# Kernel tuning notes

Hardware: AMD Instinct MI355X
Metric: run time of the kernel (lower is better)

## Reference

```python
import jax, jax.numpy as jnp
import numpy as np

B, L = 32, 96
N = B * L
E = B * L * L
HID, LAT, EEMB = 128, 64, 32
NLAYERS = 3
LAMBDA_CONTRAST = 0.05


def _sinusoidal(t, dim):
    half = dim // 2
    freqs = jnp.exp(-jnp.log(10000.0) * jnp.arange(half, dtype=jnp.float32) / (half - 1))
    ang = t[:, None] * freqs[None, :]
    return jnp.concatenate([jnp.sin(ang), jnp.cos(ang)], axis=-1)


def _forward(H_0, X_0, H_1, X_1, cond_embedding, t_graph,
             Wi1, bi1, Wi2, bi2, Wi3, bi3, edge_table,
             We1, be1, We2, be2, Wx, Wh1, bh1, Wh2, bh2, Wout, bout,
             edges, chain_ids, generate_mask, lengths, shift):
    n = H_0.shape[0]
    b = lengths.shape[0]
    batch_ids = jnp.repeat(jnp.arange(b), lengths, total_repeat_length=n)
    t = t_graph[batch_ids]                      # (N,)
    mask = generate_mask
    mask_f = mask.astype(jnp.float32)

    # path interpolation
    tH = t[:, None]
    H_t = jnp.where(mask[:, None], (1.0 - tH) * H_0 + tH * H_1, H_1)
    X_t = jnp.where(mask[:, None], (1.0 - tH) * X_0 + tH * X_1, X_1)
    v_H_target = H_1 - H_0
    v_X_target = X_1 - X_0

    # edge types from chain-id masking (irregular gather)
    row, col = edges[0], edges[1]
    edge_types = (chain_ids[row] != chain_ids[col]).astype(jnp.int32)

    # --- velocity net ---
    t_embed = _sinusoidal(t, HID)
    h = jnp.concatenate([H_t, cond_embedding, t_embed], axis=-1)
    h = jax.nn.relu(h @ Wi1 + bi1)
    h = jax.nn.relu(h @ Wi2 + bi2)
    h = h @ Wi3 + bi3                            # (N, HID)
    eemb = edge_table[edge_types]                # (E, EEMB)

    X = X_t
    for l in range(NLAYERS):
        rel = X[row] - X[col]                    # (E, 3)
        d2 = jnp.sum(rel * rel, axis=-1, keepdims=True)
        ef = jnp.concatenate([h[row], h[col], d2, eemb], axis=-1)
        m = jax.nn.silu(ef @ We1[l] + be1[l])
        m = jax.nn.silu(m @ We2[l] + be2[l])     # (E, HID)
        coef = m @ Wx[l]                         # (E, 1)
        X = X + jax.ops.segment_sum(rel * coef, row, num_segments=n)
        agg = jax.ops.segment_sum(m, row, num_segments=n)
        hh = jnp.concatenate([h, agg], axis=-1)
        h = h + jax.nn.silu(hh @ Wh1[l] + bh1[l]) @ Wh2[l] + bh2[l]

    v_X_pred = jnp.where(mask[:, None], X, 0.0)
    v_H_pred = jnp.where(mask[:, None], h @ Wout + bout, 0.0)

    # --- losses ---
    msum = mask_f.sum() + 1e-8
    def masked_mse(pred, tgt):
        return (jnp.sum((pred - tgt) ** 2, axis=-1) * mask_f).sum() / msum
    loss_H_pos = masked_mse(v_H_pred, v_H_target)
    loss_X_pos = masked_mse(v_X_pred, v_X_target)

    # negatives: roll over node dim (matches torch indexing (arange+shift)%N)
    v_H_target_neg = jnp.roll(H_1, -shift, axis=0) - jnp.roll(H_0, -shift, axis=0)
    v_X_target_neg = jnp.roll(X_1, -shift, axis=0) - jnp.roll(X_0, -shift, axis=0)
    loss_H_neg = masked_mse(v_H_pred, v_H_target_neg)
    loss_X_neg = masked_mse(v_X_pred, v_X_target_neg)

    loss_H = loss_H_pos - LAMBDA_CONTRAST * loss_H_neg
    loss_X = loss_X_pos - LAMBDA_CONTRAST * loss_X_neg
    return jnp.stack([loss_H, loss_X, loss_H_pos, loss_X_pos, loss_H_neg, loss_X_neg])


def setup_inputs() -> dict:
    key = jax.random.key(0)
    ks = iter(jax.random.split(key, 40))
    def nrm(shape, fan_in):
        return jax.random.normal(next(ks), shape, dtype=jnp.float32) / np.sqrt(fan_in)

    # all-pairs edges within each graph (uniform lengths)
    idx = np.arange(L)
    rb, cb = np.repeat(idx, L), np.tile(idx, L)
    off = (np.arange(B) * L)[:, None]
    rows = (off + rb[None, :]).reshape(-1)
    cols = (off + cb[None, :]).reshape(-1)
    edges = jnp.asarray(np.stack([rows, cols]).astype(np.int32))

    d_in_mlp = LAT + 2 * HID       # 320
    d_in_e = 2 * HID + 1 + EEMB    # 289
    inp = {
        "H_0": jax.random.normal(next(ks), (N, LAT), dtype=jnp.float32),
        "X_0": jax.random.normal(next(ks), (N, 3), dtype=jnp.float32),
        "H_1": jax.random.normal(next(ks), (N, LAT), dtype=jnp.float32),
        "X_1": jax.random.normal(next(ks), (N, 3), dtype=jnp.float32),
        "cond_embedding": jax.random.normal(next(ks), (N, HID), dtype=jnp.float32),
        "t_graph": jax.random.uniform(next(ks), (B,), dtype=jnp.float32),
        "Wi1": nrm((d_in_mlp, HID), d_in_mlp), "bi1": jnp.zeros((HID,)),
        "Wi2": nrm((HID, HID), HID), "bi2": jnp.zeros((HID,)),
        "Wi3": nrm((HID, HID), HID), "bi3": jnp.zeros((HID,)),
        "edge_table": jax.random.normal(next(ks), (2, EEMB), dtype=jnp.float32),
        "We1": nrm((NLAYERS, d_in_e, HID), d_in_e), "be1": jnp.zeros((NLAYERS, HID)),
        "We2": nrm((NLAYERS, HID, HID), HID), "be2": jnp.zeros((NLAYERS, HID)),
        "Wx": nrm((NLAYERS, HID, 1), HID) * 0.01,
        "Wh1": nrm((NLAYERS, 2 * HID, HID), 2 * HID), "bh1": jnp.zeros((NLAYERS, HID)),
        "Wh2": nrm((NLAYERS, HID, HID), HID), "bh2": jnp.zeros((NLAYERS, HID)),
        "Wout": nrm((HID, LAT), HID), "bout": jnp.zeros((LAT,)),
        "edges": edges,
        "chain_ids": jax.random.randint(next(ks), (N,), 0, 3).astype(jnp.int32),
        "generate_mask": jax.random.bernoulli(next(ks), 0.5, (N,)),
        "lengths": jnp.full((B,), L, dtype=jnp.int32),
        "shift": 7,
    }
    return inp


def reference(H_0, X_0, H_1, X_1, cond_embedding, t_graph,
              Wi1, bi1, Wi2, bi2, Wi3, bi3, edge_table,
              We1, be1, We2, be2, Wx, Wh1, bh1, Wh2, bh2, Wout, bout,
              edges, chain_ids, generate_mask, lengths, shift):
    return _forward(H_0, X_0, H_1, X_1, cond_embedding, t_graph,
                    Wi1, bi1, Wi2, bi2, Wi3, bi3, edge_table,
                    We1, be1, We2, be2, Wx, Wh1, bh1, Wh2, bh2, Wout, bout,
                    edges, chain_ids, generate_mask, lengths, shift)
```

## Files before the change

kernel.cpp:

```cpp
#include <hip/hip_runtime.h>
#include <hip/hip_bf16.h>
#include <math.h>

#define NBATCH 32
#define LSEQ   96
#define NN     3072
#define HID    128
#define LAT    64
#define EEMB   32

#define OFF_H      0
#define OFF_X      (OFF_H   + NN*HID)
#define OFF_PA     (OFF_X   + NN*3)
#define OFF_AGG    (OFF_PA  + NN*HID)
#define OFF_DX     (OFF_AGG + NN*HID)
#define OFF_ET     (OFF_DX  + NN*3)
#define OFF_ACC    (OFF_ET  + 768)
#define OFF_NBID   (OFF_ACC + 8)
#define OFF_CUM    (OFF_NBID + NN)
#define OFF_PBH    (OFF_CUM + 40)
#define OFF_BPE    (OFF_PBH + NN*HID/2)
#define OFF_BAB    (OFF_BPE + 24576)
#define OFF_BH1    (OFF_BAB + 49152)
#define OFF_BH2    (OFF_BH1 + 49152)
#define OFF_BWO    (OFF_BH2 + 24576)
#define OFF_BWI1   (OFF_BWO + 4096)
#define OFF_BWI2   (OFF_BWI1 + 20480)
#define OFF_BWI3   (OFF_BWI2 + 8192)
#define OFF_CNT    (OFF_BWI3 + 8192)

typedef short bf16x8 __attribute__((ext_vector_type(8)));
typedef float f32x4  __attribute__((ext_vector_type(4)));

__device__ __forceinline__ short f2bf(float f) {
    unsigned u = __builtin_bit_cast(unsigned, f);
    unsigned r = (u + 0x7FFFu + ((u >> 16) & 1u)) >> 16;
    return (short)r;
}
__device__ __forceinline__ short2 f2bf2(float a, float b) {
    __hip_bfloat162 h = __float22bfloat162_rn(make_float2(a, b));
    short2 r;
    __builtin_memcpy(&r, &h, sizeof(r));
    return r;
}
__device__ __forceinline__ float bf2f(short s) {
    unsigned u = ((unsigned)(unsigned short)s) << 16;
    return __builtin_bit_cast(float, u);
}
__device__ __forceinline__ float silu(float z) {
    return z * __builtin_amdgcn_rcpf(1.0f + __expf(-z));
}

__global__ void k0_all(const float* __restrict__ edge_table, const float* __restrict__ We1,
                       const int* __restrict__ lengths, const float* __restrict__ We2,
                       const float* __restrict__ Wh1, const float* __restrict__ Wh2,
                       const float* __restrict__ Wout, const float* __restrict__ Wi1,
                       const float* __restrict__ Wi2, const float* __restrict__ Wi3,
                       float* __restrict__ ws) {
    int tid = threadIdx.x;
    if (blockIdx.x == 1472) {
        int* cum = (int*)(ws + OFF_CUM);
        int* nb  = (int*)(ws + OFF_NBID);
        float* et = ws + OFF_ET;
        if (tid == 0) {
            int s = 0;
            for (int b = 0; b < NBATCH; b++) { cum[b] = s; s += lengths[b]; }
            cum[NBATCH] = s;
        }
        if (tid < 8) ws[OFF_ACC + tid] = 0.0f;
        if (tid < 128) ((unsigned*)(ws + OFF_CNT))[tid] = 0u;
        __syncthreads();
        for (int i = tid; i < NN; i += blockDim.x) {
            int b = NBATCH - 1;
            for (int q = 0; q < NBATCH; q++) { if (i < cum[q + 1]) { b = q; break; } }
            nb[i] = b;
        }
        for (int idx = tid; idx < 3 * 2 * HID; idx += blockDim.x) {
            int c = idx & 127;
            int t = (idx >> 7) & 1;
            int l = idx >> 8;
            const float* w = We1 + (l * 289 + 257) * HID + c;
            const float* e = edge_table + t * EEMB;
            float s = 0.f;
            for (int k = 0; k < EEMB; k++) s += e[k] * w[k * HID];
            et[idx] = s;
        }
        return;
    }
    int idx = blockIdx.x * 256 + tid;
    short* bpe  = (short*)(ws + OFF_BPE);
    short* bab  = (short*)(ws + OFF_BAB);
    short* bh1  = (short*)(ws + OFF_BH1);
    short* bh2  = (short*)(ws + OFF_BH2);
    short* bwo  = (short*)(ws + OFF_BWO);
    short* bwi1 = (short*)(ws + OFF_BWI1);
    short* bwi2 = (short*)(ws + OFF_BWI2);
    short* bwi3 = (short*)(ws + OFF_BWI3);
    if (idx < 49152) {
        int k = idx & 127, n = (idx >> 7) & 127, l = idx >> 14;
        bpe[idx] = f2bf(We2[(l * 128 + k) * 128 + n]);
    } else if (idx < 147456) {
        int q = idx - 49152;
        int k = q & 127, n = (q >> 7) & 255, l = q >> 15;
        float v = (n < 128) ? We1[(l * 289 + k) * 128 + n]
                            : We1[(l * 289 + 128 + k) * 128 + (n - 128)];
        bab[q] = f2bf(v);
    } else if (idx < 245760) {
        int q = idx - 147456;
        int k = q & 255, n = (q >> 8) & 127, l = q >> 15;
        bh1[q] = f2bf(Wh1[(l * 256 + k) * 128 + n]);
    } else if (idx < 294912) {
        int q = idx - 245760;
        int k = q & 127, n = (q >> 7) & 127, l = q >> 14;
        bh2[q] = f2bf(Wh2[(l * 128 + k) * 128 + n]);
    } else if (idx < 303104) {
        int q = idx - 294912;
        int k = q & 127, n = q >> 7;
        bwo[q] = f2bf(Wout[k * 64 + n]);
    } else if (idx < 344064) {
        int q = idx - 303104;
        int n = q / 320, k = q - n * 320;
        bwi1[q] = f2bf(Wi1[k * 128 + n]);
    } else if (idx < 360448) {
        int q = idx - 344064;
        int k = q & 127, n = q >> 7;
        bwi2[q] = f2bf(Wi2[k * 128 + n]);
    } else if (idx < 376832) {
        int q = idx - 360448;
        int k = q & 127, n = q >> 7;
        bwi3[q] = f2bf(Wi3[k * 128 + n]);
    }
}

__global__ void __launch_bounds__(256)
k1s_node_init(const float* __restrict__ H0, const float* __restrict__ X0,
              const float* __restrict__ H1, const float* __restrict__ X1,
              const float* __restrict__ cond, const float* __restrict__ tg,
              const float* __restrict__ bi1, const float* __restrict__ bi2,
              const float* __restrict__ bi3, const float* __restrict__ be1,
              const int* __restrict__ gmask, float* __restrict__ ws) {
    __shared__ short u1[16 * 136];
    __shared__ short u2[16 * 136];
    int rowbase = blockIdx.x * 96 + blockIdx.y * 16;
    int tid = threadIdx.x;
    int w = tid >> 6, lane = tid & 63;
    int quad = lane >> 4, lp = lane & 15;
    int nodeA = rowbase + lp;
    const int* nb = (const int*)(ws + OFF_NBID);
    float t = tg[nb[nodeA]];
    float u = (gmask[nodeA] != 0) ? t : 1.0f;

    if (tid < 48) {
        int node = rowbase + tid / 3, d = tid % 3;
        float tn = tg[nb[node]];
        float un = (gmask[node] != 0) ? tn : 1.0f;
        ws[OFF_X + (size_t)node * 3 + d] =
            (1.0f - un) * X0[(size_t)node * 3 + d] + un * X1[(size_t)node * 3 + d];
    }

    const short* bwi1 = (const short*)(ws + OFF_BWI1);
    const short* bwi2 = (const short*)(ws + OFF_BWI2);
    const short* bwi3 = (const short*)(ws + OFF_BWI3);
    const short* bab  = (const short*)(ws + OFF_BAB);

    f32x4 acc[2];
    acc[0] = (f32x4){0.f, 0.f, 0.f, 0.f};
    acc[1] = (f32x4){0.f, 0.f, 0.f, 0.f};
    for (int s = 0; s < 10; s++) {
        int kb = s * 32 + quad * 8;
        float z[8];
        if (kb < 64) {
            const float* h0 = H0 + (size_t)nodeA * 64 + kb;
            const float* h1 = H1 + (size_t)nodeA * 64 + kb;
            #pragma unroll
            for (int e = 0; e < 8; e++) z[e] = (1.0f - u) * h0[e] + u * h1[e];
        } else if (kb < 192) {
            const float* cp = cond + (size_t)nodeA * 128 + (kb - 64);
            #pragma unroll
            for (int e = 0; e < 8; e++) z[e] = cp[e];
        } else if (kb < 256) {
            #pragma unroll
            for (int e = 0; e < 8; e++) {
                float c = (float)(kb - 192 + e);
                float fr = __expf(-9.2103403719761836f * c / 63.0f);
                z[e] = __sinf(t * fr);
            }
        } else {
            #pragma unroll
            for (int e = 0; e < 8; e++) {
                float c = (float)(kb - 256 + e);
                float fr = __expf(-9.2103403719761836f * c / 63.0f);
                z[e] = __cosf(t * fr);
            }
        }
        bf16x8 af;
        #pragma unroll
        for (int e = 0; e < 8; e += 2) {
            short2 p = f2bf2(z[e], z[e + 1]);
            af[e] = p.x; af[e + 1] = p.y;
        }
        #pragma unroll
        for (int i = 0; i < 2; i++) {
            int ct = 2 * w + i;
            bf16x8 bf = *(const bf16x8*)(bwi1 + (size_t)(16 * ct + lp) * 320 + kb);
            acc[i] = __builtin_amdgcn_mfma_f32_16x16x32_bf16(af, bf, acc[i], 0, 0, 0);
        }
    }
    #pragma unroll
    for (int i = 0; i < 2; i++) {
        int ch = 16 * (2 * w + i) + lp;
        float bb1 = bi1[ch];
        #pragma unroll
        for (int r = 0; r < 4; r++)
            u1[(quad * 4 + r) * 136 + ch] = f2bf(fmaxf(acc[i][r] + bb1, 0.0f));
    }
    __syncthreads();

    acc[0] = (f32x4){0.f, 0.f, 0.f, 0.f};
    acc[1] = (f32x4){0.f, 0.f, 0.f, 0.f};
    #pragma unroll
    for (int s = 0; s < 4; s++) {
        int kb = s * 32 + quad * 8;
        bf16x8 af = *(const bf16x8*)(u1 + lp * 136 + kb);
        #pragma unroll
        for (int i = 0; i < 2; i++) {
            int ct = 2 * w + i;
            bf16x8 bf = *(const bf16x8*)(bwi2 + (size_t)(16 * ct + lp) * 128 + kb);
            acc[i] = __builtin_amdgcn_mfma_f32_16x16x32_bf16(af, bf, acc[i], 0, 0, 0);
        }
    }
    #pragma unroll
    for (int i = 0; i < 2; i++) {
        int ch = 16 * (2 * w + i) + lp;
        float bb2 = bi2[ch];
        #pragma unroll
        for (int r = 0; r < 4; r++)
            u2[(quad * 4 + r) * 136 + ch] = f2bf(fmaxf(acc[i][r] + bb2, 0.0f));
    }
    __syncthreads();

    acc[0] = (f32x4){0.f, 0.f, 0.f, 0.f};
    acc[1] = (f32x4){0.f, 0.f, 0.f, 0.f};
    #pragma unroll
    for (int s = 0; s < 4; s++) {
        int kb = s * 32 + quad * 8;
        bf16x8 af = *(const bf16x8*)(u2 + lp * 136 + kb);
        #pragma unroll
        for (int i = 0; i < 2; i++) {
            int ct = 2 * w + i;
            bf16x8 bf = *(const bf16x8*)(bwi3 + (size_t)(16 * ct + lp) * 128 + kb);
            acc[i] = __builtin_amdgcn_mfma_f32_16x16x32_bf16(af, bf, acc[i], 0, 0, 0);
        }
    }
    #pragma unroll
    for (int i = 0; i < 2; i++) {
        int ch = 16 * (2 * w + i) + lp;
        float bb3 = bi3[ch];
        #pragma unroll
        for (int r = 0; r < 4; r++) {
            int row = quad * 4 + r;
            float h = acc[i][r] + bb3;
            ws[OFF_H + (size_t)(rowbase + row) * 128 + ch] = h;
            u1[row * 136 + ch] = f2bf(h);
        }
    }
    __syncthreads();

    f32x4 acc4[4];
    #pragma unroll
    for (int i = 0; i < 4; i++) acc4[i] = (f32x4){0.f, 0.f, 0.f, 0.f};
    #pragma unroll
    for (int s = 0; s < 4; s++) {
        int kb = s * 32 + quad * 8;
        bf16x8 af = *(const bf16x8*)(u1 + lp * 136 + kb);
        #pragma unroll
        for (int i = 0; i < 4; i++) {
            int ct4 = 4 * w + i;
            bf16x8 bf = *(const bf16x8*)(bab + (size_t)(16 * ct4 + lp) * 128 + kb);
            acc4[i] = __builtin_amdgcn_mfma_f32_16x16x32_bf16(af, bf, acc4[i], 0, 0, 0);
        }
    }
    short* pbh = (short*)(ws + OFF_PBH);
    #pragma unroll
    for (int i = 0; i < 4; i++) {
        int ct4 = 4 * w + i;
        #pragma unroll
        for (int r = 0; r < 4; r++) {
            int node = rowbase + quad * 4 + r;
            if (ct4 < 8) {
                int ch = 16 * ct4 + lp;
                ws[OFF_PA + (size_t)node * 128 + ch] = acc4[i][r] + be1[ch];
            } else {
                int ch = 16 * (ct4 - 8) + lp;
                pbh[(size_t)node * 128 + ch] = f2bf(acc4[i][r]);
            }
        }
    }
}

#define KG 4
#define SMC_BS    0
#define SMC_AGG   32768
#define SMC_PA    35840
#define SMC_ET    37888
#define SMC_WC    38912
#define SMC_COEF  39424
#define SMC_XT    39808
#define SMC_CI    39856
__global__ void __launch_bounds__(384)
k3c_edge(const float* __restrict__ We1, const float* __restrict__ Wx,
         const float* __restrict__ be2, const int* __restrict__ chain,
         int l, float* __restrict__ ws) {
    __shared__ __align__(16) char smem[39872];
    short* bS    = (short*)(smem + SMC_BS);
    float* aggP  = (float*)(smem + SMC_AGG);
    float* paS   = (float*)(smem + SMC_PA);
    float* etS   = (float*)(smem + SMC_ET);
    float* wcS   = (float*)(smem + SMC_WC);
    float* coefS = (float*)(smem + SMC_COEF);
    float* xT    = (float*)(smem + SMC_XT);
    int*   ciS   = (int*)  (smem + SMC_CI);

    int tid = threadIdx.x;
    int i0 = blockIdx.x * KG;
    int colbase = (i0 / 96) * 96;
    const float* Xc = ws + OFF_X;

    {
        const short* bpe = (const short*)(ws + OFF_BPE) + (size_t)l * 128 * 128;
        for (int idx = tid; idx < 2048; idx += 384) {
            int t = idx >> 8, s = (idx >> 6) & 3, ln = idx & 63;
            int lq = ln >> 4, lpp = ln & 15;
            *(bf16x8*)(bS + idx * 8) =
                *(const bf16x8*)(bpe + (size_t)(16 * t + lpp) * 128 + s * 32 + lq * 8);
        }
        if (tid < 128) {
            #pragma unroll
            for (int g = 0; g < KG; g++)
                paS[g * 128 + tid] = ws[OFF_PA + (size_t)(i0 + g) * 128 + tid];
            etS[tid]       = ws[OFF_ET + l * 256 + tid];
            etS[128 + tid] = ws[OFF_ET + l * 256 + 128 + tid];
            wcS[tid]       = We1[(l * 289 + 256) * 128 + tid];
        }
        if (tid < KG * 3) xT[tid] = Xc[(size_t)(i0 + tid / 3) * 3 + tid % 3];
        if (tid < KG) ciS[tid] = chain[i0 + tid];
    }

    int w = tid >> 6, lane = tid & 63;
    int quad = lane >> 4, lp = lane & 15;
    int jA = 16 * w + lp;
    const short* pbrow = (const short*)(ws + OFF_PBH) + (size_t)(colbase + jA) * 128;
    bf16x8 pbv[4];
    #pragma unroll
    for (int s = 0; s < 4; s++) pbv[s] = *(const bf16x8*)(pbrow + s * 32 + quad * 8);
    float xr0 = Xc[(size_t)(colbase + jA) * 3 + 0];
    float xr1 = Xc[(size_t)(colbase + jA) * 3 + 1];
    float xr2 = Xc[(size_t)(colbase + jA) * 3 + 2];
    int cj = chain[colbase + jA];
    float be2r[8], wxr[8];
    #pragma unroll
    for (int t = 0; t < 8; t++) {
        int ch = 16 * t + lp;
        be2r[t] = be2[l * 128 + ch];
        wxr[t]  = Wx[l * 128 + ch];
    }
    float ex0 = 0.f, ex1 = 0.f;
    if (w < 3) {
        ex0 = Xc[(size_t)(colbase + lane) * 3 + w];
        if (lane < 32) ex1 = Xc[(size_t)(colbase + lane + 64) * 3 + w];
    }
    __syncthreads();

    for (int g = 0; g < KG; g++) {
        float rx = xT[g * 3 + 0] - xr0;
        float ry = xT[g * 3 + 1] - xr1;
        float rz = xT[g * 3 + 2] - xr2;
        float d2j = rx * rx + ry * ry + rz * rz;
        const float* etP = etS + ((cj != ciS[g]) ? 128 : 0);
        const float* paP = paS + g * 128;

        f32x4 acc[8];
        #pragma unroll
        for (int t = 0; t < 8; t++) acc[t] = (f32x4){0.f, 0.f, 0.f, 0.f};

        #pragma unroll
        for (int s = 0; s < 4; s++) {
            int kb = s * 32 + quad * 8;
            float z[8];
            #pragma unroll
            for (int e = 0; e < 8; e++)
                z[e] = silu(paP[kb + e] + etP[kb + e] + bf2f(pbv[s][e]) + d2j * wcS[kb + e]);
            bf16x8 af;
            #pragma unroll
            for (int e = 0; e < 8; e += 2) {
                short2 p = f2bf2(z[e], z[e + 1]);
                af[e] = p.x; af[e + 1] = p.y;
            }
            #pragma unroll
            for (int t = 0; t < 8; t++) {
                bf16x8 bf = *(const bf16x8*)(bS + ((t * 4 + s) * 64 + lane) * 8);
                acc[t] = __builtin_amdgcn_mfma_f32_16x16x32_bf16(af, bf, acc[t], 0, 0, 0);
            }
        }

        float cp[4] = {0.f, 0.f, 0.f, 0.f};
        #pragma unroll
        for (int t = 0; t < 8; t++) {
            float ag = 0.f;
            #pragma unroll
            for (int r = 0; r < 4; r++) {
                float m2 = silu(acc[t][r] + be2r[t]);
                ag += m2;
                cp[r] += m2 * wxr[t];
            }
            ag += __shfl_xor(ag, 16);
            ag += __shfl_xor(ag, 32);
            if (lane < 16) aggP[w * 128 + 16 * t + lp] = ag;
        }
        #pragma unroll
        for (int r = 0; r < 4; r++) {
            float v = cp[r];
            v += __shfl_xor(v, 1);
            v += __shfl_xor(v, 2);
            v += __shfl_xor(v, 4);
            v += __shfl_xor(v, 8);
            if (lp == 0) coefS[16 * w + quad * 4 + r] = v;
        }
        __syncthreads();

        if (tid < 128) {
            float s = 0.f;
            #pragma unroll
            for (int q = 0; q < 6; q++) s += aggP[q * 128 + tid];
            ws[OFF_AGG + (size_t)(i0 + g) * 128 + tid] = s;
        }
        if (w < 3) {
            float v = (xT[g * 3 + w] - ex0) * coefS[lane];
            if (lane < 32) v += (xT[g * 3 + w] - ex1) * coefS[lane + 64];
            #pragma unroll
            for (int o = 32; o > 0; o >>= 1) v += __shfl_down(v, o);
            if (lane == 0) ws[OFF_DX + (size_t)(i0 + g) * 3 + w] = v;
        }
        __syncthreads();
    }
}

__global__ void __launch_bounds__(256)
k4s_node_post(const float* __restrict__ bh1, const float* __restrict__ bh2,
              const float* __restrict__ be1, const float* __restrict__ bout,
              const float* __restrict__ H0, const float* __restrict__ X0,
              const float* __restrict__ H1, const float* __restrict__ X1,
              const int* __restrict__ gmask, const int* __restrict__ shiftp,
              int l, float* __restrict__ ws, float* __restrict__ out) {
    __shared__ short uS[16 * 136];
    __shared__ short hS[16 * 136];
    __shared__ float redE[4], redN[4];
    __shared__ float sxp, sxn, scnt;
    int rowbase = blockIdx.x * 96 + blockIdx.y * 16;
    int tid = threadIdx.x;
    int w = tid >> 6, lane = tid & 63;
    int quad = lane >> 4, lp = lane & 15;
    int nodeA = rowbase + lp;
    const short* b1 = (const short*)(ws + OFF_BH1) + (size_t)l * 128 * 256;
    const short* b2 = (const short*)(ws + OFF_BH2) + (size_t)l * 128 * 128;

    if (tid == 0) { sxp = 0.f; sxn = 0.f; scnt = 0.f; }
    if (tid < 48) {
        int node = rowbase + tid / 3, d = tid % 3;
        ws[OFF_X + (size_t)node * 3 + d] += ws[OFF_DX + (size_t)node * 3 + d];
    }

    f32x4 acc[2];
    acc[0] = (f32x4){0.f, 0.f, 0.f, 0.f};
    acc[1] = (f32x4){0.f, 0.f, 0.f, 0.f};
    #pragma unroll
    for (int s = 0; s < 8; s++) {
        int kb = s * 32 + quad * 8;
        const float* src = (kb < 128) ? (ws + OFF_H + (size_t)nodeA * 128 + kb)
                                      : (ws + OFF_AGG + (size_t)nodeA * 128 + (kb - 128));
        bf16x8 af;
        #pragma unroll
        for (int e = 0; e < 8; e += 2) {
            short2 p = f2bf2(src[e], src[e + 1]);
            af[e] = p.x; af[e + 1] = p.y;
        }
        #pragma unroll
        for (int i = 0; i < 2; i++) {
            int ct = 2 * w + i;
            bf16x8 bf = *(const bf16x8*)(b1 + (size_t)(16 * ct + lp) * 256 + kb);
            acc[i] = __builtin_amdgcn_mfma_f32_16x16x32_bf16(af, bf, acc[i], 0, 0, 0);
        }
    }
    #pragma unroll
    for (int i = 0; i < 2; i++) {
        int ch = 16 * (2 * w + i) + lp;
        float bb1 = bh1[l * 128 + ch];
        #pragma unroll
        for (int r = 0; r < 4; r++)
            uS[(quad * 4 + r) * 136 + ch] = f2bf(silu(acc[i][r] + bb1));
    }
    __syncthreads();

    acc[0] = (f32x4){0.f, 0.f, 0.f, 0.f};
    acc[1] = (f32x4){0.f, 0.f, 0.f, 0.f};
    #pragma unroll
    for (int s = 0; s < 4; s++) {
        int kb = s * 32 + quad * 8;
        bf16x8 af = *(const bf16x8*)(uS + lp * 136 + kb);
        #pragma unroll
        for (int i = 0; i < 2; i++) {
            int ct = 2 * w + i;
            bf16x8 bf = *(const bf16x8*)(b2 + (size_t)(16 * ct + lp) * 128 + kb);
            acc[i] = __builtin_amdgcn_mfma_f32_16x16x32_bf16(af, bf, acc[i], 0, 0, 0);
        }
    }
    #pragma unroll
    for (int i = 0; i < 2; i++) {
        int ch = 16 * (2 * w + i) + lp;
        float bb2 = bh2[l * 128 + ch];
        #pragma unroll
        for (int r = 0; r < 4; r++) {
            int row = quad * 4 + r;
            size_t off = OFF_H + (size_t)(rowbase + row) * 128 + ch;
            float h = ws[off] + acc[i][r] + bb2;
            ws[off] = h;
            hS[row * 136 + ch] = f2bf(h);
        }
    }
    __syncthreads();

    if (l < 2) {
        const short* bab = (const short*)(ws + OFF_BAB) + (size_t)(l + 1) * 256 * 128;
        f32x4 acc4[4];
        #pragma unroll
        for (int i = 0; i < 4; i++) acc4[i] = (f32x4){0.f, 0.f, 0.f, 0.f};
        #pragma unroll
        for (int s = 0; s < 4; s++) {
            int kb = s * 32 + quad * 8;
            bf16x8 af = *(const bf16x8*)(hS + lp * 136 + kb);
            #pragma unroll
            for (int i = 0; i < 4; i++) {
                int ct4 = 4 * w + i;
                bf16x8 bf = *(const bf16x8*)(bab + (size_t)(16 * ct4 + lp) * 128 + kb);
                acc4[i] = __builtin_amdgcn_mfma_f32_16x16x32_bf16(af, bf, acc4[i], 0, 0, 0);
            }
        }
        short* pbh = (short*)(ws + OFF_PBH);
        #pragma unroll
        for (int i = 0; i < 4; i++) {
            int ct4 = 4 * w + i;
            #pragma unroll
            for (int r = 0; r < 4; r++) {
                int node = rowbase + quad * 4 + r;
                if (ct4 < 8) {
                    int ch = 16 * ct4 + lp;
                    ws[OFF_PA + (size_t)node * 128 + ch] = acc4[i][r] + be1[(l + 1) * 128 + ch];
                } else {
                    int ch = 16 * (ct4 - 8) + lp;
                    pbh[(size_t)node * 128 + ch] = f2bf(acc4[i][r]);
                }
            }
        }
    } else {
        const short* bwo = (const short*)(ws + OFF_BWO);
        f32x4 accv = (f32x4){0.f, 0.f, 0.f, 0.f};
        #pragma unroll
        for (int s = 0; s < 4; s++) {
            int kb = s * 32 + quad * 8;
            bf16x8 af = *(const bf16x8*)(hS + lp * 136 + kb);
            bf16x8 bf = *(const bf16x8*)(bwo + (size_t)(16 * w + lp) * 128 + kb);
            accv = __builtin_amdgcn_mfma_f32_16x16x32_bf16(af, bf, accv, 0, 0, 0);
        }
        int s = shiftp[0] % NN; if (s < 0) s += NN;
        int col = 16 * w + lp;
        float bo = bout[col];
        float ep = 0.f, en = 0.f;
        #pragma unroll
        for (int r = 0; r < 4; r++) {
            int row = rowbase + quad * 4 + r;
            if (gmask[row] != 0) {
                int ip = row + s; if (ip >= NN) ip -= NN;
                float v  = accv[r] + bo;
                float tp = H1[(size_t)row * 64 + col] - H0[(size_t)row * 64 + col];
                float tn = H1[(size_t)ip * 64 + col]  - H0[(size_t)ip * 64 + col];
                float dp = v - tp, dn = v - tn;
                ep += dp * dp;
                en += dn * dn;
            }
        }
        #pragma unroll
        for (int o = 1; o < 64; o <<= 1) {
            ep += __shfl_xor(ep, o);
            en += __shfl_xor(en, o);
        }
        if (lane == 0) { redE[w] = ep; redN[w] = en; }

        if (tid < 16) {
            int node = rowbase + tid;
            if (gmask[node] != 0) {
                int ip = node + s; if (ip >= NN) ip -= NN;
                float xp = 0.f, xn = 0.f;
                #pragma unroll
                for (int d = 0; d < 3; d++) {
                    float xv  = ws[OFF_X + (size_t)node * 3 + d];
                    float tpx = X1[(size_t)node * 3 + d] - X0[(size_t)node * 3 + d];
                    float tnx = X1[(size_t)ip * 3 + d]   - X0[(size_t)ip * 3 + d];
                    xp += (xv - tpx) * (xv - tpx);
                    xn += (xv - tnx) * (xv - tnx);
                }
                atomicAdd(&sxp, xp);
                atomicAdd(&sxn, xn);
                atomicAdd(&scnt, 1.0f);
            }
        }
        __syncthreads();
        if (tid == 0) {
            float eT = redE[0] + redE[1] + redE[2] + redE[3];
            float nT = redN[0] + redN[1] + redN[2] + redN[3];
            float* acc0 = ws + OFF_ACC;
            atomicAdd(acc0 + 0, eT);
            atomicAdd(acc0 + 2, nT);
            atomicAdd(acc0 + 1, sxp);
            atomicAdd(acc0 + 3, sxn);
            atomicAdd(acc0 + 4, scnt);
            __threadfence();
            unsigned o2 = atomicAdd((unsigned*)(ws + OFF_CNT) + 96, 1u);
            if (o2 == 191u) {
                __threadfence();
                float a0 = atomicAdd(acc0 + 0, 0.0f);
                float a1 = atomicAdd(acc0 + 1, 0.0f);
                float a2 = atomicAdd(acc0 + 2, 0.0f);
                float a3 = atomicAdd(acc0 + 3, 0.0f);
                float a4 = atomicAdd(acc0 + 4, 0.0f);
                float msum = a4 + 1e-8f;
                float lhp = a0 / msum, lxp = a1 / msum;
                float lhn = a2 / msum, lxn = a3 / msum;
                out[0] = lhp - 0.05f * lhn;
                out[1] = lxp - 0.05f * lxn;
                out[2] = lhp;
                out[3] = lxp;
                out[4] = lhn;
                out[5] = lxn;
            }
        }
    }
}

extern "C" void kernel_launch(void* const* d_in, const int* in_sizes, int n_in,
                              void* d_out, int out_size, void* d_ws, size_t ws_size,
                              hipStream_t stream) {
    (void)in_sizes; (void)n_in; (void)out_size; (void)ws_size;
    const float* H0   = (const float*)d_in[0];
    const float* X0   = (const float*)d_in[1];
    const float* H1   = (const float*)d_in[2];
    const float* X1   = (const float*)d_in[3];
    const float* cond = (const float*)d_in[4];
    const float* tg   = (const float*)d_in[5];
    const float* Wi1  = (const float*)d_in[6];
    const float* bi1  = (const float*)d_in[7];
    const float* Wi2  = (const float*)d_in[8];
    const float* bi2  = (const float*)d_in[9];
    const float* Wi3  = (const float*)d_in[10];
    const float* bi3  = (const float*)d_in[11];
    const float* etab = (const float*)d_in[12];
    const float* We1  = (const float*)d_in[13];
    const float* be1  = (const float*)d_in[14];
    const float* We2  = (const float*)d_in[15];
    const float* be2  = (const float*)d_in[16];
    const float* Wx   = (const float*)d_in[17];
    const float* Wh1  = (const float*)d_in[18];
    const float* bh1  = (const float*)d_in[19];
    const float* Wh2  = (const float*)d_in[20];
    const float* bh2  = (const float*)d_in[21];
    const float* Wout = (const float*)d_in[22];
    const float* bout = (const float*)d_in[23];
    const int* chain   = (const int*)d_in[25];
    const int* gmask   = (const int*)d_in[26];
    const int* lengths = (const int*)d_in[27];
    const int* shiftp  = (const int*)d_in[28];
    float* ws  = (float*)d_ws;
    float* out = (float*)d_out;

    k0_all<<<1473, 256, 0, stream>>>(etab, We1, lengths, We2, Wh1, Wh2,
                                     Wout, Wi1, Wi2, Wi3, ws);
    k1s_node_init<<<dim3(NBATCH, 6), 256, 0, stream>>>(H0, X0, H1, X1, cond, tg,
                                                       bi1, bi2, bi3, be1, gmask, ws);
    for (int l = 0; l < 3; l++) {
        k3c_edge<<<NN / KG, 384, 0, stream>>>(We1, Wx, be2, chain, l, ws);
        k4s_node_post<<<dim3(NBATCH, 6), 256, 0, stream>>>(bh1, bh2, be1, bout,
                                                           H0, X0, H1, X1, gmask, shiftp,
                                                           l, ws, out);
    }
}
```

Before: 389.7 us.

## Interleave two target nodes per edge MFMA pass and widen node-post kernel to 8 waves

The edge kernel now handles two destination nodes at once, issuing paired MFMAs that share each B-fragment load from LDS, and moves be2/Wx from per-thread registers into shared memory. The node-post kernel runs 512 threads (8 waves), so each wave computes one 16-column tile instead of two. In the final layer only the first four waves do the output projection. The aim is more instruction-level parallelism and less register pressure per wave, at the cost of doubled accumulator registers in the edge kernel and extra LDS reads.

```diff
diff --git a/kernel.cpp b/kernel.cpp
--- a/kernel.cpp
+++ b/kernel.cpp
@@ -304,19 +304,23 @@
 #define SMC_PA    35840
 #define SMC_ET    37888
 #define SMC_WC    38912
-#define SMC_COEF  39424
-#define SMC_XT    39808
-#define SMC_CI    39856
+#define SMC_BE2   39424
+#define SMC_WX    39936
+#define SMC_COEF  40448
+#define SMC_XT    40832
+#define SMC_CI    40880
 __global__ void __launch_bounds__(384)
-k3c_edge(const float* __restrict__ We1, const float* __restrict__ Wx,
-         const float* __restrict__ be2, const int* __restrict__ chain,
-         int l, float* __restrict__ ws) {
-    __shared__ __align__(16) char smem[39872];
+k3c2_edge(const float* __restrict__ We1, const float* __restrict__ Wx,
+          const float* __restrict__ be2, const int* __restrict__ chain,
+          int l, float* __restrict__ ws) {
+    __shared__ __align__(16) char smem[40896];
     short* bS    = (short*)(smem + SMC_BS);
     float* aggP  = (float*)(smem + SMC_AGG);
     float* paS   = (float*)(smem + SMC_PA);
     float* etS   = (float*)(smem + SMC_ET);
     float* wcS   = (float*)(smem + SMC_WC);
+    float* be2S  = (float*)(smem + SMC_BE2);
+    float* wxS   = (float*)(smem + SMC_WX);
     float* coefS = (float*)(smem + SMC_COEF);
     float* xT    = (float*)(smem + SMC_XT);
     int*   ciS   = (int*)  (smem + SMC_CI);
@@ -341,6 +345,8 @@
             etS[tid]       = ws[OFF_ET + l * 256 + tid];
             etS[128 + tid] = ws[OFF_ET + l * 256 + 128 + tid];
             wcS[tid]       = We1[(l * 289 + 256) * 128 + tid];
+            be2S[tid]      = be2[l * 128 + tid];
+            wxS[tid]       = Wx[l * 128 + tid];
         }
         if (tid < KG * 3) xT[tid] = Xc[(size_t)(i0 + tid / 3) * 3 + tid % 3];
         if (tid < KG) ciS[tid] = chain[i0 + tid];
@@ -357,13 +363,6 @@
     float xr1 = Xc[(size_t)(colbase + jA) * 3 + 1];
     float xr2 = Xc[(size_t)(colbase + jA) * 3 + 2];
     int cj = chain[colbase + jA];
-    float be2r[8], wxr[8];
-    #pragma unroll
-    for (int t = 0; t < 8; t++) {
-        int ch = 16 * t + lp;
-        be2r[t] = be2[l * 128 + ch];
-        wxr[t]  = Wx[l * 128 + ch];
-    }
     float ex0 = 0.f, ex1 = 0.f;
     if (w < 3) {
         ex0 = Xc[(size_t)(colbase + lane) * 3 + w];
@@ -371,90 +370,109 @@
     }
     __syncthreads();
 
-    for (int g = 0; g < KG; g++) {
-        float rx = xT[g * 3 + 0] - xr0;
-        float ry = xT[g * 3 + 1] - xr1;
-        float rz = xT[g * 3 + 2] - xr2;
-        float d2j = rx * rx + ry * ry + rz * rz;
-        const float* etP = etS + ((cj != ciS[g]) ? 128 : 0);
-        const float* paP = paS + g * 128;
-
-        f32x4 acc[8];
-        #pragma unroll
-        for (int t = 0; t < 8; t++) acc[t] = (f32x4){0.f, 0.f, 0.f, 0.f};
+    for (int gp = 0; gp < KG; gp += 2) {
+        int gA = gp, gB = gp + 1;
+        float rxA = xT[gA * 3 + 0] - xr0, ryA = xT[gA * 3 + 1] - xr1, rzA = xT[gA * 3 + 2] - xr2;
+        float rxB = xT[gB * 3 + 0] - xr0, ryB = xT[gB * 3 + 1] - xr1, rzB = xT[gB * 3 + 2] - xr2;
+        float d2A = rxA * rxA + ryA * ryA + rzA * rzA;
+        float d2B = rxB * rxB + ryB * ryB + rzB * rzB;
+        const float* etA = etS + ((cj != ciS[gA]) ? 128 : 0);
+        const float* etB = etS + ((cj != ciS[gB]) ? 128 : 0);
+        const float* paA = paS + gA * 128;
+        const float* paB = paS + gB * 128;
+
+        f32x4 accA[8], accB[8];
+        #pragma unroll
+        for (int t = 0; t < 8; t++) {
+            accA[t] = (f32x4){0.f, 0.f, 0.f, 0.f};
+            accB[t] = (f32x4){0.f, 0.f, 0.f, 0.f};
+        }
 
         #pragma unroll
         for (int s = 0; s < 4; s++) {
             int kb = s * 32 + quad * 8;
-            float z[8];
-            #pragma unroll
-            for (int e = 0; e < 8; e++)
-                z[e] = silu(paP[kb + e] + etP[kb + e] + bf2f(pbv[s][e]) + d2j * wcS[kb + e]);
-            bf16x8 af;
+            bf16x8 afA, afB;
             #pragma unroll
             for (int e = 0; e < 8; e += 2) {
-                short2 p = f2bf2(z[e], z[e + 1]);
-                af[e] = p.x; af[e + 1] = p.y;
+                float pb0 = bf2f(pbv[s][e]), pb1 = bf2f(pbv[s][e + 1]);
+                float wc0 = wcS[kb + e], wc1 = wcS[kb + e + 1];
+                float zA0 = silu(paA[kb + e]     + etA[kb + e]     + pb0 + d2A * wc0);
+                float zA1 = silu(paA[kb + e + 1] + etA[kb + e + 1] + pb1 + d2A * wc1);
+                float zB0 = silu(paB[kb + e]     + etB[kb + e]     + pb0 + d2B * wc0);
+                float zB1 = silu(paB[kb + e + 1] + etB[kb + e + 1] + pb1 + d2B * wc1);
+                short2 pA = f2bf2(zA0, zA1);
+                short2 pB = f2bf2(zB0, zB1);
+                afA[e] = pA.x; afA[e + 1] = pA.y;
+                afB[e] = pB.x; afB[e + 1] = pB.y;
             }
             #pragma unroll
             for (int t = 0; t < 8; t++) {
                 bf16x8 bf = *(const bf16x8*)(bS + ((t * 4 + s) * 64 + lane) * 8);
-                acc[t] = __builtin_amdgcn_mfma_f32_16x16x32_bf16(af, bf, acc[t], 0, 0, 0);
-            }
-        }
-
-        float cp[4] = {0.f, 0.f, 0.f, 0.f};
-        #pragma unroll
-        for (int t = 0; t < 8; t++) {
-            float ag = 0.f;
+                accA[t] = __builtin_amdgcn_mfma_f32_16x16x32_bf16(afA, bf, accA[t], 0, 0, 0);
+                accB[t] = __builtin_amdgcn_mfma_f32_16x16x32_bf16(afB, bf, accB[t], 0, 0, 0);
+            }
+        }
+
+        #pragma unroll
+        for (int half = 0; half < 2; half++) {
+            int g = (half == 0) ? gA : gB;
+            f32x4* acc = (half == 0) ? accA : accB;
+            float cp[4] = {0.f, 0.f, 0.f, 0.f};
+            #pragma unroll
+            for (int t = 0; t < 8; t++) {
+                int ch = 16 * t + lp;
+                float bb = be2S[ch];
+                float wx = wxS[ch];
+                float ag = 0.f;
+                #pragma unroll
+                for (int r = 0; r < 4; r++) {
+                    float m2 = silu(acc[t][r] + bb);
+                    ag += m2;
+                    cp[r] += m2 * wx;
+                }
+                ag += __shfl_xor(ag, 16);
+                ag += __shfl_xor(ag, 32);
+                if (lane < 16) aggP[w * 128 + ch] = ag;
+            }
             #pragma unroll
             for (int r = 0; r < 4; r++) {
-                float m2 = silu(acc[t][r] + be2r[t]);
-                ag += m2;
-                cp[r] += m2 * wxr[t];
-            }
-            ag += __shfl_xor(ag, 16);
-            ag += __shfl_xor(ag, 32);
-            if (lane < 16) aggP[w * 128 + 16 * t + lp] = ag;
-        }
-        #pragma unroll
-        for (int r = 0; r < 4; r++) {
-            float v = cp[r];
-            v += __shfl_xor(v, 1);
-            v += __shfl_xor(v, 2);
-            v += __shfl_xor(v, 4);
-            v += __shfl_xor(v, 8);
-            if (lp == 0) coefS[16 * w + quad * 4 + r] = v;
-        }
-        __syncthreads();
-
-        if (tid < 128) {
-            float s = 0.f;
-            #pragma unroll
-            for (int q = 0; q < 6; q++) s += aggP[q * 128 + tid];
-            ws[OFF_AGG + (size_t)(i0 + g) * 128 + tid] = s;
-        }
-        if (w < 3) {
-            float v = (xT[g * 3 + w] - ex0) * coefS[lane];
-            if (lane < 32) v += (xT[g * 3 + w] - ex1) * coefS[lane + 64];
-            #pragma unroll
-            for (int o = 32; o > 0; o >>= 1) v += __shfl_down(v, o);
-            if (lane == 0) ws[OFF_DX + (size_t)(i0 + g) * 3 + w] = v;
-        }
-        __syncthreads();
-    }
-}
-
-__global__ void __launch_bounds__(256)
-k4s_node_post(const float* __restrict__ bh1, const float* __restrict__ bh2,
-              const float* __restrict__ be1, const float* __restrict__ bout,
-              const float* __restrict__ H0, const float* __restrict__ X0,
-              const float* __restrict__ H1, const float* __restrict__ X1,
-              const int* __restrict__ gmask, const int* __restrict__ shiftp,
-              int l, float* __restrict__ ws, float* __restrict__ out) {
+                float v = cp[r];
+                v += __shfl_xor(v, 1);
+                v += __shfl_xor(v, 2);
+                v += __shfl_xor(v, 4);
+                v += __shfl_xor(v, 8);
+                if (lp == 0) coefS[16 * w + quad * 4 + r] = v;
+            }
+            __syncthreads();
+
+            if (tid < 128) {
+                float s = 0.f;
+                #pragma unroll
+                for (int q = 0; q < 6; q++) s += aggP[q * 128 + tid];
+                ws[OFF_AGG + (size_t)(i0 + g) * 128 + tid] = s;
+            }
+            if (w < 3) {
+                float v = (xT[g * 3 + w] - ex0) * coefS[lane];
+                if (lane < 32) v += (xT[g * 3 + w] - ex1) * coefS[lane + 64];
+                #pragma unroll
+                for (int o = 32; o > 0; o >>= 1) v += __shfl_down(v, o);
+                if (lane == 0) ws[OFF_DX + (size_t)(i0 + g) * 3 + w] = v;
+            }
+            __syncthreads();
+        }
+    }
+}
+
+__global__ void __launch_bounds__(512)
+k4s8_node_post(const float* __restrict__ bh1, const float* __restrict__ bh2,
+               const float* __restrict__ be1, const float* __restrict__ bout,
+               const float* __restrict__ H0, const float* __restrict__ X0,
+               const float* __restrict__ H1, const float* __restrict__ X1,
+               const int* __restrict__ gmask, const int* __restrict__ shiftp,
+               int l, float* __restrict__ ws, float* __restrict__ out) {
     __shared__ short uS[16 * 136];
     __shared__ short hS[16 * 136];
-    __shared__ float redE[4], redN[4];
+    __shared__ float redE[8], redN[8];
     __shared__ float sxp, sxn, scnt;
     int rowbase = blockIdx.x * 96 + blockIdx.y * 16;
     int tid = threadIdx.x;
@@ -470,9 +488,7 @@
         ws[OFF_X + (size_t)node * 3 + d] += ws[OFF_DX + (size_t)node * 3 + d];
     }
 
-    f32x4 acc[2];
-    acc[0] = (f32x4){0.f, 0.f, 0.f, 0.f};
-    acc[1] = (f32x4){0.f, 0.f, 0.f, 0.f};
+    f32x4 acc = (f32x4){0.f, 0.f, 0.f, 0.f};
     #pragma unroll
     for (int s = 0; s < 8; s++) {
         int kb = s * 32 + quad * 8;
@@ -484,45 +500,34 @@
             short2 p = f2bf2(src[e], src[e + 1]);
             af[e] = p.x; af[e + 1] = p.y;
         }
-        #pragma unroll
-        for (int i = 0; i < 2; i++) {
-            int ct = 2 * w + i;
-            bf16x8 bf = *(const bf16x8*)(b1 + (size_t)(16 * ct + lp) * 256 + kb);
-            acc[i] = __builtin_amdgcn_mfma_f32_16x16x32_bf16(af, bf, acc[i], 0, 0, 0);
-        }
-    }
-    #pragma unroll
-    for (int i = 0; i < 2; i++) {
-        int ch = 16 * (2 * w + i) + lp;
+        bf16x8 bf = *(const bf16x8*)(b1 + (size_t)(16 * w + lp) * 256 + kb);
+        acc = __builtin_amdgcn_mfma_f32_16x16x32_bf16(af, bf, acc, 0, 0, 0);
+    }
+    {
+        int ch = 16 * w + lp;
         float bb1 = bh1[l * 128 + ch];
         #pragma unroll
         for (int r = 0; r < 4; r++)
-            uS[(quad * 4 + r) * 136 + ch] = f2bf(silu(acc[i][r] + bb1));
+            uS[(quad * 4 + r) * 136 + ch] = f2bf(silu(acc[r] + bb1));
     }
     __syncthreads();
 
-    acc[0] = (f32x4){0.f, 0.f, 0.f, 0.f};
-    acc[1] = (f32x4){0.f, 0.f, 0.f, 0.f};
+    acc = (f32x4){0.f, 0.f, 0.f, 0.f};
     #pragma unroll
     for (int s = 0; s < 4; s++) {
         int kb = s * 32 + quad * 8;
         bf16x8 af = *(const bf16x8*)(uS + lp * 136 + kb);
-        #pragma unroll
-        for (int i = 0; i < 2; i++) {
-            int ct = 2 * w + i;
-            bf16x8 bf = *(const bf16x8*)(b2 + (size_t)(16 * ct + lp) * 128 + kb);
-            acc[i] = __builtin_amdgcn_mfma_f32_16x16x32_bf16(af, bf, acc[i], 0, 0, 0);
-        }
-    }
-    #pragma unroll
-    for (int i = 0; i < 2; i++) {
-        int ch = 16 * (2 * w + i) + lp;
+        bf16x8 bf = *(const bf16x8*)(b2 + (size_t)(16 * w + lp) * 128 + kb);
+        acc = __builtin_amdgcn_mfma_f32_16x16x32_bf16(af, bf, acc, 0, 0, 0);
+    }
+    {
+        int ch = 16 * w + lp;
         float bb2 = bh2[l * 128 + ch];
         #pragma unroll
         for (int r = 0; r < 4; r++) {
             int row = quad * 4 + r;
             size_t off = OFF_H + (size_t)(rowbase + row) * 128 + ch;
-            float h = ws[off] + acc[i][r] + bb2;
+            float h = ws[off] + acc[r] + bb2;
             ws[off] = h;
             hS[row * 136 + ch] = f2bf(h);
         }
@@ -531,24 +536,24 @@
 
     if (l < 2) {
         const short* bab = (const short*)(ws + OFF_BAB) + (size_t)(l + 1) * 256 * 128;
-        f32x4 acc4[4];
-        #pragma unroll
-        for (int i = 0; i < 4; i++) acc4[i] = (f32x4){0.f, 0.f, 0.f, 0.f};
+        f32x4 acc4[2];
+        acc4[0] = (f32x4){0.f, 0.f, 0.f, 0.f};
+        acc4[1] = (f32x4){0.f, 0.f, 0.f, 0.f};
         #pragma unroll
         for (int s = 0; s < 4; s++) {
             int kb = s * 32 + quad * 8;
             bf16x8 af = *(const bf16x8*)(hS + lp * 136 + kb);
             #pragma unroll
-            for (int i = 0; i < 4; i++) {
-                int ct4 = 4 * w + i;
+            for (int i = 0; i < 2; i++) {
+                int ct4 = 2 * w + i;
                 bf16x8 bf = *(const bf16x8*)(bab + (size_t)(16 * ct4 + lp) * 128 + kb);
                 acc4[i] = __builtin_amdgcn_mfma_f32_16x16x32_bf16(af, bf, acc4[i], 0, 0, 0);
             }
         }
         short* pbh = (short*)(ws + OFF_PBH);
         #pragma unroll
-        for (int i = 0; i < 4; i++) {
-            int ct4 = 4 * w + i;
+        for (int i = 0; i < 2; i++) {
+            int ct4 = 2 * w + i;
             #pragma unroll
             for (int r = 0; r < 4; r++) {
                 int node = rowbase + quad * 4 + r;
@@ -563,37 +568,39 @@
         }
     } else {
         const short* bwo = (const short*)(ws + OFF_BWO);
-        f32x4 accv = (f32x4){0.f, 0.f, 0.f, 0.f};
-        #pragma unroll
-        for (int s = 0; s < 4; s++) {
-            int kb = s * 32 + quad * 8;
-            bf16x8 af = *(const bf16x8*)(hS + lp * 136 + kb);
-            bf16x8 bf = *(const bf16x8*)(bwo + (size_t)(16 * w + lp) * 128 + kb);
-            accv = __builtin_amdgcn_mfma_f32_16x16x32_bf16(af, bf, accv, 0, 0, 0);
-        }
         int s = shiftp[0] % NN; if (s < 0) s += NN;
-        int col = 16 * w + lp;
-        float bo = bout[col];
         float ep = 0.f, en = 0.f;
-        #pragma unroll
-        for (int r = 0; r < 4; r++) {
-            int row = rowbase + quad * 4 + r;
-            if (gmask[row] != 0) {
-                int ip = row + s; if (ip >= NN) ip -= NN;
-                float v  = accv[r] + bo;
-                float tp = H1[(size_t)row * 64 + col] - H0[(size_t)row * 64 + col];
-                float tn = H1[(size_t)ip * 64 + col]  - H0[(size_t)ip * 64 + col];
-                float dp = v - tp, dn = v - tn;
-                ep += dp * dp;
-                en += dn * dn;
-            }
-        }
-        #pragma unroll
-        for (int o = 1; o < 64; o <<= 1) {
-            ep += __shfl_xor(ep, o);
-            en += __shfl_xor(en, o);
-        }
-        if (lane == 0) { redE[w] = ep; redN[w] = en; }
+        if (w < 4) {
+            f32x4 accv = (f32x4){0.f, 0.f, 0.f, 0.f};
+            #pragma unroll
+            for (int ss = 0; ss < 4; ss++) {
+                int kb = ss * 32 + quad * 8;
+                bf16x8 af = *(const bf16x8*)(hS + lp * 136 + kb);
+                bf16x8 bf = *(const bf16x8*)(bwo + (size_t)(16 * w + lp) * 128 + kb);
+                accv = __builtin_amdgcn_mfma_f32_16x16x32_bf16(af, bf, accv, 0, 0, 0);
+            }
+            int col = 16 * w + lp;
+            float bo = bout[col];
+            #pragma unroll
+            for (int r = 0; r < 4; r++) {
+                int row = rowbase + quad * 4 + r;
+                if (gmask[row] != 0) {
+                    int ip = row + s; if (ip >= NN) ip -= NN;
+                    float v  = accv[r] + bo;
+                    float tp = H1[(size_t)row * 64 + col] - H0[(size_t)row * 64 + col];
+                    float tn = H1[(size_t)ip * 64 + col]  - H0[(size_t)ip * 64 + col];
+                    float dp = v - tp, dn = v - tn;
+                    ep += dp * dp;
+                    en += dn * dn;
+                }
+            }
+            #pragma unroll
+            for (int o = 1; o < 64; o <<= 1) {
+                ep += __shfl_xor(ep, o);
+                en += __shfl_xor(en, o);
+            }
+        }
+        if (lane == 0) { redE[w] = (w < 4) ? ep : 0.f; redN[w] = (w < 4) ? en : 0.f; }
 
         if (tid < 16) {
             int node = rowbase + tid;
@@ -615,8 +622,9 @@
         }
         __syncthreads();
         if (tid == 0) {
-            float eT = redE[0] + redE[1] + redE[2] + redE[3];
-            float nT = redN[0] + redN[1] + redN[2] + redN[3];
+            float eT = 0.f, nT = 0.f;
+            #pragma unroll
+            for (int q = 0; q < 8; q++) { eT += redE[q]; nT += redN[q]; }
             float* acc0 = ws + OFF_ACC;
             atomicAdd(acc0 + 0, eT);
             atomicAdd(acc0 + 2, nT);
@@ -686,9 +694,9 @@
     k1s_node_init<<<dim3(NBATCH, 6), 256, 0, stream>>>(H0, X0, H1, X1, cond, tg,
                                                        bi1, bi2, bi3, be1, gmask, ws);
     for (int l = 0; l < 3; l++) {
-        k3c_edge<<<NN / KG, 384, 0, stream>>>(We1, Wx, be2, chain, l, ws);
-        k4s_node_post<<<dim3(NBATCH, 6), 256, 0, stream>>>(bh1, bh2, be1, bout,
-                                                           H0, X0, H1, X1, gmask, shiftp,
-                                                           l, ws, out);
-    }
-}
+        k3c2_edge<<<NN / KG, 384, 0, stream>>>(We1, Wx, be2, chain, l, ws);
+        k4s8_node_post<<<dim3(NBATCH, 6), 512, 0, stream>>>(bh1, bh2, be1, bout,
+                                                            H0, X0, H1, X1, gmask, shiftp,
+                                                            l, ws, out);
+    }
+}
```

Measured after the change: 412.7 us. +5.9%, slower.
